# Kernel optimization log

Measured on AMD Instinct MI355X. Metric: run time of the kernel, lower is better.

The kernel has to match this reference:

```python
import jax, jax.numpy as jnp
import numpy as np

N = 16777216  # sequence length
C = 2         # binary BUY/SELL classes


def setup_inputs() -> dict:
    key = jax.random.key(0)
    k1, k2 = jax.random.split(key)
    inputs = jax.random.normal(k1, (N, C), dtype=jnp.float32)
    labels = jax.random.randint(k2, (N,), 0, 2, dtype=jnp.int64)
    return {"inputs": inputs, "labels": labels}


def _trend_segment_weights(labels):
    """weights[i] = remaining length (inclusive) until end of current run of equal labels.

    next_change[i] = next_change[i+1] + 1 if labels[i]==labels[i+1] else 0, next_change[-1]=0.
    Vectorized as a reversed running count of consecutive Trues, implemented via
    cummax of the last reset index (O(N), no sequential Python loop).
    """
    n = labels.shape[0]
    # e[i] = True iff labels[i] == labels[i+1]; e[n-1] = False
    e = jnp.concatenate([labels[:-1] == labels[1:], jnp.zeros((1,), dtype=bool)])
    f = e[::-1]
    r = jnp.arange(n, dtype=jnp.int32)
    # index of most recent False at or before position j
    last_false = jax.lax.cummax(jnp.where(f, jnp.int32(-1), r))
    count = r - last_false            # run length of Trues ending at j (0 if f[j] False)
    next_change = count[::-1]
    return (next_change + 1).astype(jnp.float32)


def reference(inputs, labels):
    # per-element cross entropy with logits (N, 2)
    logp = jax.nn.log_softmax(inputs, axis=-1)                      # (N, 2)
    ce = -jnp.take_along_axis(logp, labels[:, None], axis=-1)[:, 0]  # (N,)
    weights = _trend_segment_weights(labels)                         # (N,)
    return jnp.mean(ce * weights)
```

## Files before the change

kernel.cpp:

```cpp
#include <hip/hip_runtime.h>

#define N_ELEM 16777216
#define K 32
#define BLOCK 256
#define TILE (BLOCK * K)
#define NBLK (N_ELEM / TILE)
#define PAD 33
#define INV_N (1.0 / (double)N_ELEM)

__global__ void k0_zero(float* __restrict__ out) { out[0] = 0.0f; }

__device__ __forceinline__ unsigned f32_to_bf16_rne(float f) {
    unsigned b = __float_as_uint(f);
    return (b + 0x7FFFu + ((b >> 16) & 1u)) >> 16;
}

__global__ __launch_bounds__(BLOCK) void k1_all(
        const float4* __restrict__ in4, const int2* __restrict__ lab2,
        const int* __restrict__ labs, float* __restrict__ out) {
    __shared__ unsigned short ce_lds[BLOCK * PAD];
    __shared__ unsigned metaS[BLOCK];
    __shared__ double wsum[BLOCK / 64];
    const int tid = threadIdx.x;
    const long long pairBase = (long long)blockIdx.x * (TILE / 2);

    #pragma unroll
    for (int j = 0; j < K / 2; ++j) {
        int p = j * BLOCK + tid;
        float4 x = in4[pairBase + p];
        int2 lv = lab2[pairBase + p];
        int l0 = lv.x, l1 = lv.y;
        float t0 = x.y - x.x;
        float d0 = l0 ? -t0 : t0;
        float ce0 = __logf(1.0f + __expf(d0));
        float t1 = x.w - x.z;
        float d1 = l1 ? -t1 : t1;
        float ce1 = __logf(1.0f + __expf(d1));
        int it = 2 * p;
        int q = it >> 5, off = it & 31;
        ce_lds[q * PAD + off]     = (unsigned short)(f32_to_bf16_rne(ce0) | ((unsigned)l0 << 15));
        ce_lds[q * PAD + off + 1] = (unsigned short)(f32_to_bf16_rne(ce1) | ((unsigned)l1 << 15));
    }
    __syncthreads();

    const int base = tid * PAD;
    float acc = 0.f, tce = 0.f;
    int c = 0, prevLab = 0, lastLab = 0, lab = 0;
    #pragma unroll
    for (int i = K - 1; i >= 0; --i) {
        unsigned u = ce_lds[base + i];
        lab = (int)(u >> 15);
        float ce = __uint_as_float((u & 0x7FFFu) << 16);
        if (i == K - 1) { c = 1; lastLab = lab; }
        else            c = (lab == prevLab) ? c + 1 : 1;
        acc = fmaf(ce, (float)c, acc);
        if (c == K - i) tce += ce;
        prevLab = lab;
    }
    metaS[tid] = (unsigned)c | ((unsigned)lab << 6) | ((unsigned)lastLab << 7);
    __syncthreads();

    long long ext = 0;
    {
        int prevLast = lastLab;
        int t = tid + 1;
        bool open = true;
        while (t < BLOCK) {
            unsigned mb = metaS[t];
            if ((int)((mb >> 6) & 1) != prevLast) { open = false; break; }
            int hb = (int)(mb & 63);
            ext += hb;
            if (hb < K) { open = false; break; }
            prevLast = (int)((mb >> 7) & 1);
            ++t;
        }
        if (open) {
            long long g = (long long)(blockIdx.x + 1) * TILE;
            while (g < N_ELEM && labs[g] == prevLast) { ++ext; ++g; }
        }
    }
    double accd = (double)acc + (double)tce * (double)ext;

    for (int o = 32; o; o >>= 1) accd += __shfl_down(accd, o);
    int wid = tid >> 6, lane = tid & 63;
    if (lane == 0) wsum[wid] = accd;
    __syncthreads();
    if (tid == 0) {
        double t = 0.0;
        for (int w = 0; w < BLOCK / 64; ++w) t += wsum[w];
        atomicAdd(out, (float)(t * INV_N));
    }
}

extern "C" void kernel_launch(void* const* d_in, const int* in_sizes, int n_in,
                              void* d_out, int out_size, void* d_ws, size_t ws_size,
                              hipStream_t stream) {
    const float* inputs = (const float*)d_in[0];
    const int* labels = (const int*)d_in[1];
    float* out = (float*)d_out;

    k0_zero<<<1, 1, 0, stream>>>(out);
    k1_all<<<NBLK, BLOCK, 0, stream>>>(
        (const float4*)inputs, (const int2*)labels, labels, out);
}
```

Before: 238.1 us.

## Load each thread's contiguous chunk into registers, dropping the LDS transpose

```diff
diff --git a/kernel.cpp b/kernel.cpp
--- a/kernel.cpp
+++ b/kernel.cpp
@@ -5,59 +5,44 @@
 #define BLOCK 256
 #define TILE (BLOCK * K)
 #define NBLK (N_ELEM / TILE)
-#define PAD 33
 #define INV_N (1.0 / (double)N_ELEM)
 
-__global__ void k0_zero(float* __restrict__ out) { out[0] = 0.0f; }
-
-__device__ __forceinline__ unsigned f32_to_bf16_rne(float f) {
-    unsigned b = __float_as_uint(f);
-    return (b + 0x7FFFu + ((b >> 16) & 1u)) >> 16;
-}
-
 __global__ __launch_bounds__(BLOCK) void k1_all(
-        const float4* __restrict__ in4, const int2* __restrict__ lab2,
+        const float4* __restrict__ in4, const int4* __restrict__ lab4,
         const int* __restrict__ labs, float* __restrict__ out) {
-    __shared__ unsigned short ce_lds[BLOCK * PAD];
     __shared__ unsigned metaS[BLOCK];
     __shared__ double wsum[BLOCK / 64];
     const int tid = threadIdx.x;
-    const long long pairBase = (long long)blockIdx.x * (TILE / 2);
+    const long long ch = (long long)blockIdx.x * BLOCK + tid;
 
+    float4 x[16];
+    int4   lv[8];
+    const float4* ip = in4 + ch * 16;
+    const int4*   lp = lab4 + ch * 8;
     #pragma unroll
-    for (int j = 0; j < K / 2; ++j) {
-        int p = j * BLOCK + tid;
-        float4 x = in4[pairBase + p];
-        int2 lv = lab2[pairBase + p];
-        int l0 = lv.x, l1 = lv.y;
-        float t0 = x.y - x.x;
-        float d0 = l0 ? -t0 : t0;
-        float ce0 = __logf(1.0f + __expf(d0));
-        float t1 = x.w - x.z;
-        float d1 = l1 ? -t1 : t1;
-        float ce1 = __logf(1.0f + __expf(d1));
-        int it = 2 * p;
-        int q = it >> 5, off = it & 31;
-        ce_lds[q * PAD + off]     = (unsigned short)(f32_to_bf16_rne(ce0) | ((unsigned)l0 << 15));
-        ce_lds[q * PAD + off + 1] = (unsigned short)(f32_to_bf16_rne(ce1) | ((unsigned)l1 << 15));
-    }
-    __syncthreads();
+    for (int j = 0; j < 16; ++j) x[j] = ip[j];
+    #pragma unroll
+    for (int j = 0; j < 8; ++j) lv[j] = lp[j];
 
-    const int base = tid * PAD;
-    float acc = 0.f, tce = 0.f;
-    int c = 0, prevLab = 0, lastLab = 0, lab = 0;
+    float acc = 0.f, tce = 0.f, cf = 0.f;
+    int prevLab = 0, lastLab = 0, firstLab = 0;
     #pragma unroll
     for (int i = K - 1; i >= 0; --i) {
-        unsigned u = ce_lds[base + i];
-        lab = (int)(u >> 15);
-        float ce = __uint_as_float((u & 0x7FFFu) << 16);
-        if (i == K - 1) { c = 1; lastLab = lab; }
-        else            c = (lab == prevLab) ? c + 1 : 1;
-        acc = fmaf(ce, (float)c, acc);
-        if (c == K - i) tce += ce;
-        prevLab = lab;
+        float a = (i & 1) ? x[i >> 1].z : x[i >> 1].x;
+        float b = (i & 1) ? x[i >> 1].w : x[i >> 1].y;
+        int m = i & 3, l;
+        { int4 q = lv[i >> 2];
+          l = (m == 0) ? q.x : (m == 1) ? q.y : (m == 2) ? q.z : q.w; }
+        float d = l ? (a - b) : (b - a);
+        float ce = __logf(1.0f + __expf(d));
+        if (i == K - 1) { cf = 1.f; lastLab = l; }
+        else            cf = (l == prevLab) ? cf + 1.f : 1.f;
+        acc = fmaf(ce, cf, acc);
+        if (cf == (float)(K - i)) tce += ce;
+        prevLab = l;
+        firstLab = l;
     }
-    metaS[tid] = (unsigned)c | ((unsigned)lab << 6) | ((unsigned)lastLab << 7);
+    metaS[tid] = (unsigned)cf | ((unsigned)firstLab << 6) | ((unsigned)lastLab << 7);
     __syncthreads();
 
     long long ext = 0;
@@ -86,9 +71,9 @@
     if (lane == 0) wsum[wid] = accd;
     __syncthreads();
     if (tid == 0) {
-        double t = 0.0;
-        for (int w = 0; w < BLOCK / 64; ++w) t += wsum[w];
-        atomicAdd(out, (float)(t * INV_N));
+        double s = 0.0;
+        for (int w = 0; w < BLOCK / 64; ++w) s += wsum[w];
+        atomicAdd(out, (float)(s * INV_N));
     }
 }
 
@@ -99,7 +84,7 @@
     const int* labels = (const int*)d_in[1];
     float* out = (float*)d_out;
 
-    k0_zero<<<1, 1, 0, stream>>>(out);
+    hipMemsetAsync(out, 0, sizeof(float), stream);
     k1_all<<<NBLK, BLOCK, 0, stream>>>(
-        (const float4*)inputs, (const int2*)labels, labels, out);
+        (const float4*)inputs, (const int4*)labels, labels, out);
 }
```

Measured after the change: 239.8 us. No clear change (+0.7%).
